# Kernel optimization log

Hardware: AMD Instinct MI355X
Metric: run time of the kernel (lower is better)

Reference implementation:

```python
import jax, jax.numpy as jnp
import numpy as np

DISCOUNT_FACTOR = 0.99
EPS = 1e-8


def setup_inputs() -> dict:
    key = jax.random.key(0)
    k1, k2, k3 = jax.random.split(key, 3)
    B, S = 8192, 1024
    # raw params initialized exactly like the torch module: atanh(target)
    raw_gamma = jnp.arctanh(jnp.array([DISCOUNT_FACTOR], dtype=jnp.float32))
    # create_init_lambda_sequence(0.5, S): linear ramp with mean == AVERAGE_LAMBDA
    lam_init = jnp.linspace(0.1, 0.9, S).astype(jnp.float32)
    raw_lambd = jnp.arctanh(lam_init)
    values = jax.random.normal(k1, (B, S + 1, 1), dtype=jnp.float32)
    rewards = jax.random.normal(k2, (B, S, 1), dtype=jnp.float32)
    dones = jax.random.randint(k3, (B, S, 1), 0, 2).astype(jnp.int32)
    return {
        "raw_gamma": raw_gamma,
        "raw_lambd": raw_lambd,
        "values": values,
        "rewards": rewards,
        "dones": dones,
        "input_seq_len": 1024,
    }


def reference(raw_gamma, raw_lambd, values, rewards, dones, input_seq_len):
    # gamma / lambd properties: tanh then clamp_min(1e-8)
    gamma = jnp.maximum(jnp.tanh(raw_gamma), EPS)[0]            # scalar
    lambd = jnp.maximum(jnp.tanh(raw_lambd), EPS)               # [max_seq_len]
    lam_seq = lambd[-input_seq_len:]                            # [S]

    # ---- update_sum_reward_weights (runs under no_grad in torch) ----
    # backward recurrence: v[t] = gamma * (1 - lam[t] + lam[t] * v[t+1]),  v[S] = 1
    def w_step(v_next, lam_t):
        v_t = gamma * (1.0 - lam_t + lam_t * v_next)
        return v_t, jnp.maximum(1.0 - v_t, EPS)

    _, w = jax.lax.scan(
        w_step,
        jnp.asarray(1.0, values.dtype),
        jax.lax.stop_gradient(lam_seq),
        reverse=True,
    )  # w: [S]
    srw = w / jnp.maximum(w.mean(), EPS)
    sum_reward_weights = jax.lax.stop_gradient(srw)[None, :, None]  # [1, S, 1]

    # ---- calculate_lambda_returns ----
    # ret[t] = r[t] + gamma*(1-done[t]) * ((1-lam[t])*V[t+1] + lam[t]*ret[t+1])
    d = dones.astype(values.dtype)
    v_next = values[:, 1:, :]                                   # [B, S, 1]
    xs = (
        jnp.swapaxes(rewards, 0, 1),   # [S, B, 1]
        jnp.swapaxes(d, 0, 1),         # [S, B, 1]
        jnp.swapaxes(v_next, 0, 1),    # [S, B, 1]
        lam_seq,                       # [S]
    )

    def r_step(ret_next, x):
        r, dn, vn, lam = x
        ret = r + gamma * (1.0 - dn) * ((1.0 - lam) * vn + lam * ret_next)
        return ret, ret

    _, rets = jax.lax.scan(r_step, values[:, -1, :], xs, reverse=True)  # [S, B, 1]
    lambda_returns = jnp.swapaxes(rets, 0, 1)                           # [B, S, 1]
    return lambda_returns, sum_reward_weights
```

## Files before the change

### kernel.cpp

```cpp
#include <hip/hip_runtime.h>
#include <math.h>

#define EPSF 1e-8f

typedef float fvec4 __attribute__((ext_vector_type(4), aligned(4)));
typedef float nvec4 __attribute__((ext_vector_type(4)));

__device__ __forceinline__ void suffix_scan64(float& A, float& B, int lane) {
#pragma unroll
    for (int d = 1; d < 64; d <<= 1) {
        float Ao = __shfl_down(A, d);
        float Bo = __shfl_down(B, d);
        if (lane + d < 64) {
            A = fmaf(B, Ao, A);
            B = B * Bo;
        }
    }
}

__global__ __launch_bounds__(256, 8)
void td_kernel(const float* __restrict__ raw_gamma,
               const float* __restrict__ raw_lambd, int lam_off,
               const float* __restrict__ values,
               const float* __restrict__ rewards,
               const int* __restrict__ dones,
               float* __restrict__ out,
               int B, int S, int rowBlocks)
{
    __shared__ float s_gl[1024];
    __shared__ float sA[2][4], sB[2][4];
    const float gamma = fmaxf(tanhf(raw_gamma[0]), EPSF);
    for (int t = threadIdx.x; t < S; t += 256)
        s_gl[t] = gamma * fmaxf(tanhf(raw_lambd[lam_off + t]), EPSF);
    __syncthreads();

    const int lane = threadIdx.x & 63;
    const int c    = threadIdx.x >> 6;

    if ((int)blockIdx.x == rowBlocks) {
        if (threadIdx.x >= 64) return;
        const int base = lane << 4;
        float a[16], b[16];
#pragma unroll
        for (int j = 0; j < 16; ++j) { b[j] = s_gl[base + j]; a[j] = gamma - b[j]; }
        float A = a[15], Bc = b[15];
#pragma unroll
        for (int j = 14; j >= 0; --j) { A = fmaf(b[j], A, a[j]); Bc *= b[j]; }
        suffix_scan64(A, Bc, lane);
        float EA = __shfl_down(A, 1);
        float EB = __shfl_down(Bc, 1);
        if (lane == 63) { EA = 0.0f; EB = 1.0f; }
        float v = EA + EB;
        float w[16], sum = 0.0f;
#pragma unroll
        for (int j = 15; j >= 0; --j) {
            v = fmaf(b[j], v, a[j]);
            w[j] = fmaxf(1.0f - v, EPSF);
            sum += w[j];
        }
#pragma unroll
        for (int d = 32; d; d >>= 1) sum += __shfl_xor(sum, d);
        float inv = 1.0f / fmaxf(sum / (float)S, EPSF);
        float* srw = out + (size_t)B * S;
#pragma unroll
        for (int j = 0; j < 16; ++j) srw[base + j] = w[j] * inv;
        return;
    }

    const int t0 = (c << 8) + (lane << 2);
    const float4 G1 = *(const float4*)&s_gl[t0];
    const float g1v[4] = {G1.x, G1.y, G1.z, G1.w};
    const float g0v[4] = {gamma - G1.x, gamma - G1.y, gamma - G1.z, gamma - G1.w};

    float4 cr; int4 cd; fvec4 cv; float cvS;
    {
        const int r = blockIdx.x;
        cr  = *(const float4*)(rewards + (size_t)r * S + t0);
        cd  = *(const int4*)(dones + (size_t)r * S + t0);
        cv  = *(const fvec4*)(values + (size_t)r * (S + 1) + t0 + 1);
        cvS = values[(size_t)r * (S + 1) + S];
    }

    int p = 0;
#pragma unroll 1
    for (int r = blockIdx.x; r < B; r += rowBlocks) {
        const int rn = r + rowBlocks;
        float4 nr; int4 nd; fvec4 nv; float nvS = 0.0f;
        if (rn < B) {
            nr  = *(const float4*)(rewards + (size_t)rn * S + t0);
            nd  = *(const int4*)(dones + (size_t)rn * S + t0);
            nv  = *(const fvec4*)(values + (size_t)rn * (S + 1) + t0 + 1);
            nvS = values[(size_t)rn * (S + 1) + S];
        }

        float vn[4] = {cv.x, cv.y, cv.z, cv.w};
        float rr[4] = {cr.x, cr.y, cr.z, cr.w};
        int   di[4] = {cd.x, cd.y, cd.z, cd.w};
        float a[4], b[4];
#pragma unroll
        for (int j = 0; j < 4; ++j) {
            float ndn = 1.0f - (float)di[j];
            b[j] = g1v[j] * ndn;
            a[j] = fmaf(g0v[j] * vn[j], ndn, rr[j]);
        }

        float A = a[3], Bc = b[3];
#pragma unroll
        for (int j = 2; j >= 0; --j) { A = fmaf(b[j], A, a[j]); Bc *= b[j]; }
        suffix_scan64(A, Bc, lane);
        float EA = __shfl_down(A, 1);
        float EB = __shfl_down(Bc, 1);
        if (lane == 63) { EA = 0.0f; EB = 1.0f; }
        if (lane == 0) { sA[p][c] = A; sB[p][c] = Bc; }
        __syncthreads();

        float x = cvS;
#pragma unroll
        for (int j = 3; j >= 1; --j)
            if (j > c) x = fmaf(sB[p][j], x, sA[p][j]);

        float xi = fmaf(EB, x, EA);
        float o3 = fmaf(b[3], xi, a[3]);
        float o2 = fmaf(b[2], o3, a[2]);
        float o1 = fmaf(b[1], o2, a[1]);
        float o0 = fmaf(b[0], o1, a[0]);
        nvec4 ov = {o0, o1, o2, o3};
        __builtin_nontemporal_store(ov, (nvec4*)(out + (size_t)r * S + t0));

        if (rn < B) { cr = nr; cd = nd; cv = nv; cvS = nvS; }
        p ^= 1;
    }
}

extern "C" void kernel_launch(void* const* d_in, const int* in_sizes, int n_in,
                              void* d_out, int out_size, void* d_ws, size_t ws_size,
                              hipStream_t stream) {
    const float* raw_gamma = (const float*)d_in[0];
    const float* raw_lambd = (const float*)d_in[1];
    const float* values    = (const float*)d_in[2];
    const float* rewards   = (const float*)d_in[3];
    const int*   dones     = (const int*)d_in[4];
    float* out = (float*)d_out;

    int n_v = in_sizes[2];
    int n_r = in_sizes[3];
    int B = n_v - n_r;
    int S = n_r / B;
    int lam_off = in_sizes[1] - S;

    int rowBlocks = 2048;
    if (rowBlocks > B) rowBlocks = B;
    td_kernel<<<rowBlocks + 1, 256, 0, stream>>>(
        raw_gamma, raw_lambd, lam_off, values, rewards, dones,
        out, B, S, rowBlocks);
}
```

Before: 142.7 us.

## Split gamma-lambda prep into separate kernel and use one-row-per-block aligned loads

```diff
diff --git a/kernel.cpp b/kernel.cpp
--- a/kernel.cpp
+++ b/kernel.cpp
@@ -3,8 +3,12 @@
 
 #define EPSF 1e-8f
 
-typedef float fvec4 __attribute__((ext_vector_type(4), aligned(4)));
 typedef float nvec4 __attribute__((ext_vector_type(4)));
+typedef int   nivec4 __attribute__((ext_vector_type(4)));
+
+__device__ __forceinline__ float pick(nvec4 v, int i) {
+    return i == 0 ? v.x : i == 1 ? v.y : i == 2 ? v.z : v.w;
+}
 
 __device__ __forceinline__ void suffix_scan64(float& A, float& B, int lane) {
 #pragma unroll
@@ -18,118 +22,129 @@
     }
 }
 
-__global__ __launch_bounds__(256, 8)
-void td_kernel(const float* __restrict__ raw_gamma,
-               const float* __restrict__ raw_lambd, int lam_off,
-               const float* __restrict__ values,
-               const float* __restrict__ rewards,
-               const int* __restrict__ dones,
-               float* __restrict__ out,
-               int B, int S, int rowBlocks)
+__global__ __launch_bounds__(256)
+void prep_kernel(const float* __restrict__ raw_gamma,
+                 const float* __restrict__ raw_lambd, int lam_off,
+                 float* __restrict__ gl, float* __restrict__ srw, int S)
 {
     __shared__ float s_gl[1024];
-    __shared__ float sA[2][4], sB[2][4];
     const float gamma = fmaxf(tanhf(raw_gamma[0]), EPSF);
-    for (int t = threadIdx.x; t < S; t += 256)
-        s_gl[t] = gamma * fmaxf(tanhf(raw_lambd[lam_off + t]), EPSF);
+    for (int t = threadIdx.x; t < S; t += 256) {
+        float g1 = gamma * fmaxf(tanhf(raw_lambd[lam_off + t]), EPSF);
+        gl[t] = g1;
+        s_gl[t] = g1;
+    }
+    if (threadIdx.x == 0) gl[S] = gamma;
+    __syncthreads();
+    if (threadIdx.x >= 64) return;
+    const int lane = threadIdx.x;
+    const int base = lane << 4;
+    float a[16], b[16];
+#pragma unroll
+    for (int j = 0; j < 16; ++j) { b[j] = s_gl[base + j]; a[j] = gamma - b[j]; }
+    float A = a[15], Bc = b[15];
+#pragma unroll
+    for (int j = 14; j >= 0; --j) { A = fmaf(b[j], A, a[j]); Bc *= b[j]; }
+    suffix_scan64(A, Bc, lane);
+    float EA = __shfl_down(A, 1);
+    float EB = __shfl_down(Bc, 1);
+    if (lane == 63) { EA = 0.0f; EB = 1.0f; }
+    float v = EA + EB;
+    float w[16], sum = 0.0f;
+#pragma unroll
+    for (int j = 15; j >= 0; --j) {
+        v = fmaf(b[j], v, a[j]);
+        w[j] = fmaxf(1.0f - v, EPSF);
+        sum += w[j];
+    }
+#pragma unroll
+    for (int d = 32; d; d >>= 1) sum += __shfl_xor(sum, d);
+    float inv = 1.0f / fmaxf(sum / (float)S, EPSF);
+#pragma unroll
+    for (int j = 0; j < 16; ++j) srw[base + j] = w[j] * inv;
+}
+
+__global__ __launch_bounds__(256, 8)
+void td_main(const float* __restrict__ gl,
+             const float* __restrict__ values,
+             const float* __restrict__ rewards,
+             const int* __restrict__ dones,
+             float* __restrict__ out, int B, int S)
+{
+    __shared__ float sA[4], sB[4];
+    const int lane = threadIdx.x & 63;
+    const int c    = threadIdx.x >> 6;
+    const int r    = blockIdx.x;
+    const int C    = S >> 2;
+    const int t0   = c * C + (lane << 2);
+
+    const float4 G1  = *(const float4*)(gl + t0);
+    const float gamma = gl[S];
+
+    const size_t rb = (size_t)r * (S + 1);
+
+    nvec4  r4 = __builtin_nontemporal_load((const nvec4*)(rewards + (size_t)r * S + t0));
+    nivec4 d4 = __builtin_nontemporal_load((const nivec4*)(dones + (size_t)r * S + t0));
+
+    const int sh = (r + 1) & 3;
+    const size_t E  = rb + (size_t)c * C + 1;
+    const size_t A0 = E - sh;
+    nvec4 m4 = __builtin_nontemporal_load((const nvec4*)(values + A0) + lane);
+    size_t A0t = A0 + 256;
+    const size_t last4 = (size_t)B * (S + 1) - 4;
+    if (A0t > last4) A0t = last4;
+    nvec4 t4 = __builtin_nontemporal_load((const nvec4*)(values + A0t));
+    const int delta = (int)(A0 + 256 - A0t);
+    float vS = values[rb + S];
+
+    float n0 = __shfl_down(m4.x, 1);
+    float n1 = __shfl_down(m4.y, 1);
+    float n2 = __shfl_down(m4.z, 1);
+    if (lane == 63) {
+        n0 = pick(t4, delta);
+        n1 = pick(t4, delta + 1 > 3 ? 3 : delta + 1);
+        n2 = pick(t4, delta + 2 > 3 ? 3 : delta + 2);
+    }
+    float vn0, vn1, vn2, vn3;
+    if (sh == 0)      { vn0 = m4.x; vn1 = m4.y; vn2 = m4.z; vn3 = m4.w; }
+    else if (sh == 1) { vn0 = m4.y; vn1 = m4.z; vn2 = m4.w; vn3 = n0; }
+    else if (sh == 2) { vn0 = m4.z; vn1 = m4.w; vn2 = n0;   vn3 = n1; }
+    else              { vn0 = m4.w; vn1 = n0;   vn2 = n1;   vn3 = n2; }
+
+    float vn[4] = {vn0, vn1, vn2, vn3};
+    float rr[4] = {r4.x, r4.y, r4.z, r4.w};
+    int   di[4] = {d4.x, d4.y, d4.z, d4.w};
+    float g1v[4] = {G1.x, G1.y, G1.z, G1.w};
+    float a[4], b[4];
+#pragma unroll
+    for (int j = 0; j < 4; ++j) {
+        float ndn = 1.0f - (float)di[j];
+        b[j] = g1v[j] * ndn;
+        a[j] = fmaf((gamma - g1v[j]) * vn[j], ndn, rr[j]);
+    }
+
+    float A = a[3], Bc = b[3];
+#pragma unroll
+    for (int j = 2; j >= 0; --j) { A = fmaf(b[j], A, a[j]); Bc *= b[j]; }
+    suffix_scan64(A, Bc, lane);
+    float EA = __shfl_down(A, 1);
+    float EB = __shfl_down(Bc, 1);
+    if (lane == 63) { EA = 0.0f; EB = 1.0f; }
+    if (lane == 0) { sA[c] = A; sB[c] = Bc; }
     __syncthreads();
 
-    const int lane = threadIdx.x & 63;
-    const int c    = threadIdx.x >> 6;
+    float x = vS;
+#pragma unroll
+    for (int j = 3; j >= 1; --j)
+        if (j > c) x = fmaf(sB[j], x, sA[j]);
 
-    if ((int)blockIdx.x == rowBlocks) {
-        if (threadIdx.x >= 64) return;
-        const int base = lane << 4;
-        float a[16], b[16];
-#pragma unroll
-        for (int j = 0; j < 16; ++j) { b[j] = s_gl[base + j]; a[j] = gamma - b[j]; }
-        float A = a[15], Bc = b[15];
-#pragma unroll
-        for (int j = 14; j >= 0; --j) { A = fmaf(b[j], A, a[j]); Bc *= b[j]; }
-        suffix_scan64(A, Bc, lane);
-        float EA = __shfl_down(A, 1);
-        float EB = __shfl_down(Bc, 1);
-        if (lane == 63) { EA = 0.0f; EB = 1.0f; }
-        float v = EA + EB;
-        float w[16], sum = 0.0f;
-#pragma unroll
-        for (int j = 15; j >= 0; --j) {
-            v = fmaf(b[j], v, a[j]);
-            w[j] = fmaxf(1.0f - v, EPSF);
-            sum += w[j];
-        }
-#pragma unroll
-        for (int d = 32; d; d >>= 1) sum += __shfl_xor(sum, d);
-        float inv = 1.0f / fmaxf(sum / (float)S, EPSF);
-        float* srw = out + (size_t)B * S;
-#pragma unroll
-        for (int j = 0; j < 16; ++j) srw[base + j] = w[j] * inv;
-        return;
-    }
-
-    const int t0 = (c << 8) + (lane << 2);
-    const float4 G1 = *(const float4*)&s_gl[t0];
-    const float g1v[4] = {G1.x, G1.y, G1.z, G1.w};
-    const float g0v[4] = {gamma - G1.x, gamma - G1.y, gamma - G1.z, gamma - G1.w};
-
-    float4 cr; int4 cd; fvec4 cv; float cvS;
-    {
-        const int r = blockIdx.x;
-        cr  = *(const float4*)(rewards + (size_t)r * S + t0);
-        cd  = *(const int4*)(dones + (size_t)r * S + t0);
-        cv  = *(const fvec4*)(values + (size_t)r * (S + 1) + t0 + 1);
-        cvS = values[(size_t)r * (S + 1) + S];
-    }
-
-    int p = 0;
-#pragma unroll 1
-    for (int r = blockIdx.x; r < B; r += rowBlocks) {
-        const int rn = r + rowBlocks;
-        float4 nr; int4 nd; fvec4 nv; float nvS = 0.0f;
-        if (rn < B) {
-            nr  = *(const float4*)(rewards + (size_t)rn * S + t0);
-            nd  = *(const int4*)(dones + (size_t)rn * S + t0);
-            nv  = *(const fvec4*)(values + (size_t)rn * (S + 1) + t0 + 1);
-            nvS = values[(size_t)rn * (S + 1) + S];
-        }
-
-        float vn[4] = {cv.x, cv.y, cv.z, cv.w};
-        float rr[4] = {cr.x, cr.y, cr.z, cr.w};
-        int   di[4] = {cd.x, cd.y, cd.z, cd.w};
-        float a[4], b[4];
-#pragma unroll
-        for (int j = 0; j < 4; ++j) {
-            float ndn = 1.0f - (float)di[j];
-            b[j] = g1v[j] * ndn;
-            a[j] = fmaf(g0v[j] * vn[j], ndn, rr[j]);
-        }
-
-        float A = a[3], Bc = b[3];
-#pragma unroll
-        for (int j = 2; j >= 0; --j) { A = fmaf(b[j], A, a[j]); Bc *= b[j]; }
-        suffix_scan64(A, Bc, lane);
-        float EA = __shfl_down(A, 1);
-        float EB = __shfl_down(Bc, 1);
-        if (lane == 63) { EA = 0.0f; EB = 1.0f; }
-        if (lane == 0) { sA[p][c] = A; sB[p][c] = Bc; }
-        __syncthreads();
-
-        float x = cvS;
-#pragma unroll
-        for (int j = 3; j >= 1; --j)
-            if (j > c) x = fmaf(sB[p][j], x, sA[p][j]);
-
-        float xi = fmaf(EB, x, EA);
-        float o3 = fmaf(b[3], xi, a[3]);
-        float o2 = fmaf(b[2], o3, a[2]);
-        float o1 = fmaf(b[1], o2, a[1]);
-        float o0 = fmaf(b[0], o1, a[0]);
-        nvec4 ov = {o0, o1, o2, o3};
-        __builtin_nontemporal_store(ov, (nvec4*)(out + (size_t)r * S + t0));
-
-        if (rn < B) { cr = nr; cd = nd; cv = nv; cvS = nvS; }
-        p ^= 1;
-    }
+    float xi = fmaf(EB, x, EA);
+    float o3 = fmaf(b[3], xi, a[3]);
+    float o2 = fmaf(b[2], o3, a[2]);
+    float o1 = fmaf(b[1], o2, a[1]);
+    float o0 = fmaf(b[0], o1, a[0]);
+    nvec4 ov = {o0, o1, o2, o3};
+    __builtin_nontemporal_store(ov, (nvec4*)(out + (size_t)r * S + t0));
 }
 
 extern "C" void kernel_launch(void* const* d_in, const int* in_sizes, int n_in,
@@ -148,9 +163,9 @@
     int S = n_r / B;
     int lam_off = in_sizes[1] - S;
 
-    int rowBlocks = 2048;
-    if (rowBlocks > B) rowBlocks = B;
-    td_kernel<<<rowBlocks + 1, 256, 0, stream>>>(
-        raw_gamma, raw_lambd, lam_off, values, rewards, dones,
-        out, B, S, rowBlocks);
+    float* gl  = (float*)d_ws;
+    float* srw = out + (size_t)B * S;
+
+    prep_kernel<<<1, 256, 0, stream>>>(raw_gamma, raw_lambd, lam_off, gl, srw, S);
+    td_main<<<B, 256, 0, stream>>>(gl, values, rewards, dones, out, B, S);
 }
```

Measured after the change: 143.5 us. No clear change (+0.6%).
